# Kernel tuning notes

Measured on AMD Instinct MI355X. Metric: run time of the kernel, lower is better.

Reference implementation:

```python
import jax, jax.numpy as jnp
import numpy as np

B, S, D, H = 8, 4096, 512, 8
DK = D // H
DFF = 2 * D
KS = 3          # depthwise conv kernel size
EPS = 1e-6      # linear attention eps
LN_EPS = 1e-5


def setup_inputs() -> dict:
    key = jax.random.key(0)
    ks = jax.random.split(key, 24)
    w = lambda k, shape, s=0.02: (jax.random.normal(k, shape) * s).astype(jnp.float32)
    return {
        "x": jax.random.normal(ks[0], (B, S, D), dtype=jnp.float32),
        # q/k/v/o projections (torch Linear: y = x @ W.T + b, W is [out, in])
        "wq": w(ks[1], (D, D)), "bq": w(ks[2], (D,)),
        "wk": w(ks[3], (D, D)), "bk": w(ks[4], (D,)),
        "wv": w(ks[5], (D, D)), "bv": w(ks[6], (D,)),
        "wo": w(ks[7], (D, D)), "bo": w(ks[8], (D,)),
        # depthwise spatial convs on head_dim channels, weight [DK, KS], bias [DK]
        "qcw": w(ks[9], (DK, KS)), "qcb": w(ks[10], (DK,)),
        "kcw": w(ks[11], (DK, KS)), "kcb": w(ks[12], (DK,)),
        "vcw": w(ks[13], (DK, KS)), "vcb": w(ks[14], (DK,)),
        # conv-FFN 1x1 convs == linears, W1 [DFF, D], W2 [D, DFF]
        "w1": w(ks[15], (DFF, D)), "b1": w(ks[16], (DFF,)),
        "w2": w(ks[17], (D, DFF)), "b2": w(ks[18], (D,)),
        # layer norms
        "ln1_g": jnp.ones((D,), jnp.float32), "ln1_b": jnp.zeros((D,), jnp.float32),
        "ln2_g": jnp.ones((D,), jnp.float32), "ln2_b": jnp.zeros((D,), jnp.float32),
    }


def _sdwc(x, w, b):
    # x: [B, S, H, DK]; causal depthwise conv over seq per channel
    # (torch pads both sides by KS-1 then trims the last KS-1 => left pad only)
    s = x.shape[1]
    xp = jnp.pad(x, ((0, 0), (KS - 1, 0), (0, 0), (0, 0)))
    y = sum(xp[:, j:j + s] * w[:, j] for j in range(KS))
    return y + b


def _ln(x, g, b):
    m = jnp.mean(x, axis=-1, keepdims=True)
    v = jnp.mean((x - m) ** 2, axis=-1, keepdims=True)
    return (x - m) * jax.lax.rsqrt(v + LN_EPS) * g + b


def reference(x, wq, bq, wk, bk, wv, bv, qcw, qcb, kcw, kcb, vcw, vcb,
              wo, bo, w1, b1, w2, b2, ln1_g, ln1_b, ln2_g, ln2_b):
    b_, s_, _ = x.shape
    q = (jnp.einsum('bsd,od->bso', x, wq) + bq).reshape(b_, s_, H, DK)
    k = (jnp.einsum('bsd,od->bso', x, wk) + bk).reshape(b_, s_, H, DK)
    v = (jnp.einsum('bsd,od->bso', x, wv) + bv).reshape(b_, s_, H, DK)
    # depthwise spatial conv + elu(x)+1 feature map on q, k
    q = jax.nn.elu(_sdwc(q, qcw, qcb)) + 1.0
    k = jax.nn.elu(_sdwc(k, kcw, kcb)) + 1.0
    v = _sdwc(v, vcw, vcb)
    # linear attention in [B, H, S, DK]
    Q = q.transpose(0, 2, 1, 3)
    K = k.transpose(0, 2, 1, 3)
    V = v.transpose(0, 2, 1, 3)
    KV = jnp.einsum('bhsd,bhse->bhde', K, V)                       # [B,H,DK,DK]
    Z = 1.0 / jnp.einsum('bhsd,bhd->bhs', Q, K.sum(axis=2) + EPS)  # [B,H,S]
    Vn = jnp.einsum('bhde,bhsd,bhs->bhse', KV, Q, Z)               # [B,H,S,DK]
    attn = Vn.transpose(0, 2, 1, 3).reshape(b_, s_, D)
    attn = jnp.einsum('bsd,od->bso', attn, wo) + bo
    x = _ln(x + attn, ln1_g, ln1_b)
    # conv-FFN with squared (exact) GELU; dropout is identity at eval
    h = jnp.einsum('bsd,cd->bsc', x, w1) + b1
    g = jax.nn.gelu(h, approximate=False)
    h = g * g
    h = jnp.einsum('bsc,dc->bsd', h, w2) + b2
    return _ln(x + h, ln2_g, ln2_b)
```

## Files before the change

kernel.cpp:

```cpp
#include <hip/hip_runtime.h>
#include <hip/hip_bf16.h>
#include <math.h>

#define B_ 8
#define S_ 4096
#define D_ 512
#define H_ 8
#define DK_ 64
#define DFF_ 1024
#define SPLIT_ 16
#define KVSZ_ 4160
#define EPS_ 1e-6f
#define LN_EPS_ 1e-5f

typedef __attribute__((ext_vector_type(8))) short bf16x8;
typedef __attribute__((ext_vector_type(4))) float f32x4;

static __device__ __forceinline__ float b2f(unsigned short u) {
  unsigned int x = ((unsigned int)u) << 16;
  return __builtin_bit_cast(float, x);
}
static __device__ __forceinline__ unsigned short f2b(float f) {
  unsigned int u = __builtin_bit_cast(unsigned int, f);
  u += 0x7FFFu + ((u >> 16) & 1u);
  return (unsigned short)(u >> 16);
}

__global__ __launch_bounds__(256) void cvt_f32_bf16(
    const float* __restrict__ in, unsigned short* __restrict__ out, int n8)
{
  const int i = blockIdx.x * 256 + threadIdx.x;
  if (i >= n8) return;
  f32x4 a = ((const f32x4*)in)[i * 2];
  f32x4 b = ((const f32x4*)in)[i * 2 + 1];
  bf16x8 o;
  #pragma unroll
  for (int e = 0; e < 4; ++e) { o[e] = (short)f2b(a[e]); o[e + 4] = (short)f2b(b[e]); }
  ((bf16x8*)out)[i] = o;
}

__global__ __launch_bounds__(256) void cvt_weights(
    const float* __restrict__ wq, const float* __restrict__ wk,
    const float* __restrict__ wv, const float* __restrict__ wo,
    const float* __restrict__ w1, const float* __restrict__ w2,
    const float* __restrict__ bq, const float* __restrict__ bk,
    const float* __restrict__ bv,
    unsigned short* __restrict__ wb, float* __restrict__ bqkv)
{
  const int i = blockIdx.x * 256 + threadIdx.x;
  const float* src; int rel;
  if (i < 65536)       { src = (i < 32768)  ? wq : wk; rel = i & 32767; }
  else if (i < 131072) { src = (i < 98304)  ? wv : wo; rel = (i - 65536) & 32767; }
  else                 { src = (i < 196608) ? w1 : w2; rel = (i - 131072) & 65535; }
  f32x4 a = ((const f32x4*)src)[rel * 2];
  f32x4 b = ((const f32x4*)src)[rel * 2 + 1];
  bf16x8 o;
  #pragma unroll
  for (int e = 0; e < 4; ++e) { o[e] = (short)f2b(a[e]); o[e + 4] = (short)f2b(b[e]); }
  ((bf16x8*)wb)[i] = o;
  if (i < 1536) bqkv[i] = (i < 512) ? bq[i] : (i < 1024 ? bk[i - 512] : bv[i - 1024]);
}

template<int EPI>
__global__ __launch_bounds__(256, 2) void gemm_bt(
    const unsigned short* __restrict__ A,
    const unsigned short* __restrict__ W,
    const float* __restrict__ bias,
    unsigned short* __restrict__ C,
    int M, int N, int K, int ntx)
{
  __shared__ unsigned short sA[3 * 128 * 32];
  __shared__ unsigned short sB[3 * 256 * 32];
  const int t = threadIdx.x;
  const int wave = t >> 6;
  const int lane = t & 63;
  const int bid = blockIdx.x;
  const int logical = (bid & 7) * ((int)gridDim.x >> 3) + (bid >> 3);
  const int row0 = (logical / ntx) << 7;
  const int col0 = (logical % ntx) << 8;

  f32x4 acc[4][8] = {};

  const int srow = (wave << 4) + (lane >> 2);
  const int scol = (lane & 3) << 3;
  const unsigned short* ga = A + (size_t)(row0 + srow) * K + scol;
  const unsigned short* gb = W + (size_t)(col0 + srow) * K + scol;
  const int ldsoff = (wave << 9);

  const int wm = (wave >> 1) << 6;
  const int wn = (wave & 1) << 7;
  const int fr = lane & 15;
  const int fk = (lane >> 4) << 3;

  #define STAGE(bufsel, kt)                                                     \
    {                                                                           \
      _Pragma("unroll")                                                         \
      for (int i = 0; i < 2; ++i)                                               \
        __builtin_amdgcn_global_load_lds(                                       \
            (const __attribute__((address_space(1))) void*)(ga + (size_t)(i * 64) * K + (kt)), \
            (__attribute__((address_space(3))) void*)(sA + (bufsel) * 4096 + i * 2048 + ldsoff), \
            16, 0, 0);                                                          \
      _Pragma("unroll")                                                         \
      for (int i = 0; i < 4; ++i)                                               \
        __builtin_amdgcn_global_load_lds(                                       \
            (const __attribute__((address_space(1))) void*)(gb + (size_t)(i * 64) * K + (kt)), \
            (__attribute__((address_space(3))) void*)(sB + (bufsel) * 8192 + i * 2048 + ldsoff), \
            16, 0, 0);                                                          \
    }

  const int nt = K >> 5;
  STAGE(0, 0);
  STAGE(1, 32);

  int cur = 0, nxt = 2;
  for (int kt = 0; kt < nt; ++kt) {
    if (kt < nt - 1) asm volatile("s_waitcnt vmcnt(6)" ::: "memory");
    else             asm volatile("s_waitcnt vmcnt(0)" ::: "memory");
    __builtin_amdgcn_s_barrier();
    asm volatile("" ::: "memory");

    if (kt + 2 < nt) {
      STAGE(nxt, (kt + 2) * 32);
      nxt = (nxt == 2) ? 0 : nxt + 1;
    }

    const unsigned short* pA = sA + cur * 4096;
    const unsigned short* pB = sB + cur * 8192;
    bf16x8 af[4], bfv[8];
    #pragma unroll
    for (int i = 0; i < 4; ++i)
      af[i] = *(const bf16x8*)(pA + (wm + i * 16 + fr) * 32 + fk);
    #pragma unroll
    for (int j = 0; j < 8; ++j)
      bfv[j] = *(const bf16x8*)(pB + (wn + j * 16 + fr) * 32 + fk);
    #pragma unroll
    for (int i = 0; i < 4; ++i)
      #pragma unroll
      for (int j = 0; j < 8; ++j)
        acc[i][j] = __builtin_amdgcn_mfma_f32_16x16x32_bf16(af[i], bfv[j], acc[i][j], 0, 0, 0);

    cur = (cur == 2) ? 0 : cur + 1;
  }
  #undef STAGE

  const int crow0 = row0 + wm + ((lane >> 4) << 2);
  const int ccol0 = col0 + wn + fr;
  unsigned short* Cb = C;
  if (EPI == 2) Cb = C + (size_t)(col0 >> 9) * M * 512;
  const int cstride = (EPI == 2) ? 512 : N;
  #pragma unroll
  for (int j = 0; j < 8; ++j) {
    const int col = ccol0 + j * 16;
    const float bv = bias[col];
    const int lcol = (EPI == 2) ? (col & 511) : col;
    #pragma unroll
    for (int i = 0; i < 4; ++i) {
      #pragma unroll
      for (int r = 0; r < 4; ++r) {
        float v = acc[i][j][r] + bv;
        if (EPI == 1) {
          float g = 0.5f * v * (1.0f + erff(v * 0.70710678118654752f));
          v = g * g;
        }
        Cb[(size_t)(crow0 + i * 16 + r) * cstride + lcol] = f2b(v);
      }
    }
  }
}

template<bool ELUP1>
__global__ __launch_bounds__(256) void dwconv(
    const unsigned short* __restrict__ in,
    const float* __restrict__ cw,
    const float* __restrict__ cb,
    unsigned short* __restrict__ out)
{
  const int vid = blockIdx.x * 256 + threadIdx.x;
  const int d8 = vid & 63;
  const int bs = vid >> 6;
  const int s  = bs & (S_ - 1);
  const int d0 = d8 << 3;
  const int dk0 = d0 & 63;

  float acc[8], wf[3][8];
  #pragma unroll
  for (int i = 0; i < 8; ++i) acc[i] = cb[dk0 + i];
  #pragma unroll
  for (int j = 0; j < 3; ++j)
    #pragma unroll
    for (int i = 0; i < 8; ++i) wf[j][i] = cw[(dk0 + i) * 3 + j];

  const size_t base = (size_t)bs * D_ + d0;
  #pragma unroll
  for (int j = 0; j < 3; ++j) {
    const int sr = s - 2 + j;
    if (sr >= 0) {
      bf16x8 xv = *(const bf16x8*)(in + base - (size_t)(2 - j) * D_);
      #pragma unroll
      for (int i = 0; i < 8; ++i) acc[i] += wf[j][i] * b2f((unsigned short)xv[i]);
    }
  }
  bf16x8 ov;
  #pragma unroll
  for (int i = 0; i < 8; ++i) {
    float v = acc[i];
    if (ELUP1) v = (v > 0.0f) ? (v + 1.0f) : expf(v);
    ov[i] = (short)f2b(v);
  }
  *(bf16x8*)(out + base) = ov;
}

__global__ __launch_bounds__(256) void kv_partial(
    const unsigned short* __restrict__ kf,
    const unsigned short* __restrict__ vf,
    float* __restrict__ part)
{
  __shared__ unsigned short kc[16 * 64];
  __shared__ float vc[16 * 64];
  const int t = threadIdx.x;
  const int bh = blockIdx.x;
  const int b = bh >> 3, h = bh & 7;
  const int s0 = blockIdx.y * (S_ / SPLIT_);
  const int d = t >> 2;
  const int e0 = (t & 3) << 4;
  const int lr = (t & 127) >> 3;
  const int lc = (t & 7) << 3;

  float acc[16] = {};
  float ksum = 0.0f;

  for (int chunk = 0; chunk < S_ / SPLIT_; chunk += 16) {
    const size_t g = ((size_t)(b * S_ + s0 + chunk + lr)) * D_ + h * 64 + lc;
    if (t < 128) {
      *(bf16x8*)(kc + lr * 64 + lc) = *(const bf16x8*)(kf + g);
    } else {
      bf16x8 vv = *(const bf16x8*)(vf + g);
      #pragma unroll
      for (int i = 0; i < 8; ++i) vc[lr * 64 + lc + i] = b2f((unsigned short)vv[i]);
    }
    __syncthreads();
    #pragma unroll 4
    for (int ss = 0; ss < 16; ++ss) {
      const float kd = b2f(kc[ss * 64 + d]);
      ksum += kd;
      #pragma unroll
      for (int j = 0; j < 16; ++j) acc[j] += kd * vc[ss * 64 + e0 + j];
    }
    __syncthreads();
  }
  float* dst = part + ((size_t)bh * SPLIT_ + blockIdx.y) * KVSZ_;
  #pragma unroll
  for (int j = 0; j < 16; ++j) dst[d * 64 + e0 + j] = acc[j];
  if ((t & 3) == 0) dst[4096 + d] = ksum;
}

__global__ __launch_bounds__(256) void kv_finalize(
    const float* __restrict__ part, float* __restrict__ fin)
{
  const int bh = blockIdx.x;
  for (int idx = threadIdx.x; idx < KVSZ_; idx += 256) {
    float s = 0.0f;
    for (int p = 0; p < SPLIT_; ++p) s += part[((size_t)bh * SPLIT_ + p) * KVSZ_ + idx];
    if (idx >= 4096) s += EPS_;
    fin[(size_t)bh * KVSZ_ + idx] = s;
  }
}

__global__ __launch_bounds__(256) void attn_out(
    const unsigned short* __restrict__ qf,
    const float* __restrict__ fin,
    unsigned short* __restrict__ attn)
{
  __shared__ float kv[64 * 64];
  __shared__ float ks[64];
  const int t = threadIdx.x;
  const int bh = blockIdx.x, b = bh >> 3, h = bh & 7;
  const int s = blockIdx.y * 64 + (t >> 2);
  const int e0 = (t & 3) << 4;

  const float* src = fin + (size_t)bh * KVSZ_;
  for (int i = t; i < 4096; i += 256) kv[i] = src[i];
  if (t < 64) ks[t] = src[4096 + t];
  __syncthreads();

  const unsigned short* qrow = qf + ((size_t)(b * S_ + s)) * D_ + h * 64;
  float q[64];
  #pragma unroll
  for (int i = 0; i < 8; ++i) {
    bf16x8 qv = *(const bf16x8*)(qrow + i * 8);
    #pragma unroll
    for (int k = 0; k < 8; ++k) q[i * 8 + k] = b2f((unsigned short)qv[k]);
  }
  float zden = 0.0f;
  #pragma unroll
  for (int dd = 0; dd < 64; ++dd) zden += q[dd] * ks[dd];
  const float z = 1.0f / zden;

  float acc[16] = {};
  for (int dd = 0; dd < 64; ++dd) {
    const float qd = q[dd];
    #pragma unroll
    for (int j = 0; j < 16; ++j) acc[j] += qd * kv[dd * 64 + e0 + j];
  }
  unsigned short* orow = attn + ((size_t)(b * S_ + s)) * D_ + h * 64 + e0;
  bf16x8 o0, o1;
  #pragma unroll
  for (int j = 0; j < 8; ++j) { o0[j] = (short)f2b(acc[j] * z); o1[j] = (short)f2b(acc[8 + j] * z); }
  *(bf16x8*)(orow) = o0;
  *(bf16x8*)(orow + 8) = o1;
}

template<bool AF32, bool OF32>
__global__ __launch_bounds__(256) void ln_add(
    const void* __restrict__ xa_,
    const unsigned short* __restrict__ xb,
    const float* __restrict__ gg,
    const float* __restrict__ bb,
    void* __restrict__ out_)
{
  const int t = threadIdx.x, lane = t & 63, w = t >> 6;
  const size_t row = (size_t)blockIdx.x * 4 + w;
  const size_t base = row * D_ + lane * 8;

  float v[8];
  if (AF32) {
    const float* xa = (const float*)xa_;
    f32x4 a0 = *(const f32x4*)(xa + base);
    f32x4 a1 = *(const f32x4*)(xa + base + 4);
    #pragma unroll
    for (int i = 0; i < 4; ++i) { v[i] = a0[i]; v[i + 4] = a1[i]; }
  } else {
    bf16x8 a = *(const bf16x8*)((const unsigned short*)xa_ + base);
    #pragma unroll
    for (int i = 0; i < 8; ++i) v[i] = b2f((unsigned short)a[i]);
  }
  bf16x8 c = *(const bf16x8*)(xb + base);
  float sum = 0.0f;
  #pragma unroll
  for (int i = 0; i < 8; ++i) { v[i] += b2f((unsigned short)c[i]); sum += v[i]; }
  #pragma unroll
  for (int off = 1; off < 64; off <<= 1) sum += __shfl_xor(sum, off, 64);
  const float mean = sum * (1.0f / 512.0f);
  float sq = 0.0f;
  #pragma unroll
  for (int i = 0; i < 8; ++i) { const float dd = v[i] - mean; sq += dd * dd; }
  #pragma unroll
  for (int off = 1; off < 64; off <<= 1) sq += __shfl_xor(sq, off, 64);
  const float rstd = rsqrtf(sq * (1.0f / 512.0f) + LN_EPS_);

  if (OF32) {
    float* out = (float*)out_;
    f32x4 o0, o1;
    #pragma unroll
    for (int i = 0; i < 4; ++i) {
      o0[i] = (v[i] - mean) * rstd * gg[lane * 8 + i] + bb[lane * 8 + i];
      o1[i] = (v[i + 4] - mean) * rstd * gg[lane * 8 + i + 4] + bb[lane * 8 + i + 4];
    }
    *(f32x4*)(out + base) = o0;
    *(f32x4*)(out + base + 4) = o1;
  } else {
    unsigned short* out = (unsigned short*)out_;
    bf16x8 o;
    #pragma unroll
    for (int i = 0; i < 8; ++i)
      o[i] = (short)f2b((v[i] - mean) * rstd * gg[lane * 8 + i] + bb[lane * 8 + i]);
    *(bf16x8*)(out + base) = o;
  }
}

extern "C" void kernel_launch(void* const* d_in, const int* in_sizes, int n_in,
                              void* d_out, int out_size, void* d_ws, size_t ws_size,
                              hipStream_t stream) {
  const float* x    = (const float*)d_in[0];
  const float* wq   = (const float*)d_in[1];
  const float* bq   = (const float*)d_in[2];
  const float* wk   = (const float*)d_in[3];
  const float* bk   = (const float*)d_in[4];
  const float* wv   = (const float*)d_in[5];
  const float* bv   = (const float*)d_in[6];
  const float* wo   = (const float*)d_in[7];
  const float* bo   = (const float*)d_in[8];
  const float* qcw  = (const float*)d_in[9];
  const float* qcb  = (const float*)d_in[10];
  const float* kcw  = (const float*)d_in[11];
  const float* kcb  = (const float*)d_in[12];
  const float* vcw  = (const float*)d_in[13];
  const float* vcb  = (const float*)d_in[14];
  const float* w1   = (const float*)d_in[15];
  const float* b1   = (const float*)d_in[16];
  const float* w2   = (const float*)d_in[17];
  const float* b2   = (const float*)d_in[18];
  const float* ln1g = (const float*)d_in[19];
  const float* ln1b = (const float*)d_in[20];
  const float* ln2g = (const float*)d_in[21];
  const float* ln2b = (const float*)d_in[22];

  const size_t E = (size_t)B_ * S_ * D_;
  unsigned short* s0 = (unsigned short*)d_ws;
  unsigned short* s1 = s0 + E;
  unsigned short* s2 = s0 + 2 * E;
  unsigned short* s3 = s0 + 3 * E;
  float* part = (float*)s2;
  float* fin  = part + (size_t)64 * SPLIT_ * KVSZ_;

  unsigned short* wb = (unsigned short*)d_out;
  unsigned short* wqkv_b = wb;
  unsigned short* wo_b   = wb + 786432;
  unsigned short* w1_b   = wb + 1048576;
  unsigned short* w2_b   = wb + 1572864;
  float* bqkv = (float*)(wb + 2097152);

  const int M = B_ * S_;

  cvt_f32_bf16<<<(int)(E / 8 / 256), 256, 0, stream>>>(x, s3, (int)(E / 8));
  cvt_weights<<<1024, 256, 0, stream>>>(wq, wk, wv, wo, w1, w2, bq, bk, bv, wb, bqkv);

  gemm_bt<2><<<1536, 256, 0, stream>>>(s3, wqkv_b, bqkv, s0, M, 1536, D_, 6);
  dwconv<true ><<<M * 64 / 256, 256, 0, stream>>>(s0, qcw, qcb, s3);
  dwconv<true ><<<M * 64 / 256, 256, 0, stream>>>(s1, kcw, kcb, s0);
  dwconv<false><<<M * 64 / 256, 256, 0, stream>>>(s2, vcw, vcb, s1);
  kv_partial<<<dim3(B_ * H_, SPLIT_), 256, 0, stream>>>(s0, s1, part);
  kv_finalize<<<B_ * H_, 256, 0, stream>>>(part, fin);
  attn_out<<<dim3(B_ * H_, S_ / 64), 256, 0, stream>>>(s3, fin, s0);
  gemm_bt<0><<<512, 256, 0, stream>>>(s0, wo_b, bo, s1, M, D_, D_, 2);
  ln_add<true, false><<<M / 4, 256, 0, stream>>>(x, s1, ln1g, ln1b, s3);
  gemm_bt<1><<<1024, 256, 0, stream>>>(s3, w1_b, b1, s0, M, DFF_, D_, 4);
  gemm_bt<0><<<512, 256, 0, stream>>>(s0, w2_b, b2, s2, M, D_, DFF_, 2);
  ln_add<false, true><<<M / 4, 256, 0, stream>>>(s3, s2, ln2g, ln2b, d_out);
}
```

Baseline: 598.9 us.

## Fuse depthwise convs into KV and attention kernels, relax GEMM waitcnt

Removes the three standalone depthwise-conv kernels and recomputes the causal 3-tap conv (plus elu+1) inside kv_partial for K/V and inside attn_out for Q, reading pre-conv projections directly. This removes a full write and reread of three bf16 activation tensors, at the cost of loading two extra shifted rows per tile, which should mostly hit cache. The GEMM mainloop also moves its vmcnt wait to after issuing the next stage, allowing two stages in flight instead of one. Workspace buffers are reassigned so that the partial sums no longer overlap live data.

```diff
diff --git a/kernel.cpp b/kernel.cpp
--- a/kernel.cpp
+++ b/kernel.cpp
@@ -24,6 +24,9 @@
   unsigned int u = __builtin_bit_cast(unsigned int, f);
   u += 0x7FFFu + ((u >> 16) & 1u);
   return (unsigned short)(u >> 16);
+}
+static __device__ __forceinline__ float elu1(float v) {
+  return (v > 0.0f) ? (v + 1.0f) : expf(v);
 }
 
 __global__ __launch_bounds__(256) void cvt_f32_bf16(
@@ -114,14 +117,16 @@
 
   int cur = 0, nxt = 2;
   for (int kt = 0; kt < nt; ++kt) {
-    if (kt < nt - 1) asm volatile("s_waitcnt vmcnt(6)" ::: "memory");
-    else             asm volatile("s_waitcnt vmcnt(0)" ::: "memory");
     __builtin_amdgcn_s_barrier();
     asm volatile("" ::: "memory");
-
     if (kt + 2 < nt) {
       STAGE(nxt, (kt + 2) * 32);
       nxt = (nxt == 2) ? 0 : nxt + 1;
+      asm volatile("s_waitcnt vmcnt(12)" ::: "memory");
+    } else if (kt + 1 < nt) {
+      asm volatile("s_waitcnt vmcnt(6)" ::: "memory");
+    } else {
+      asm volatile("s_waitcnt vmcnt(0)" ::: "memory");
     }
 
     const unsigned short* pA = sA + cur * 4096;
@@ -168,54 +173,14 @@
   }
 }
 
-template<bool ELUP1>
-__global__ __launch_bounds__(256) void dwconv(
-    const unsigned short* __restrict__ in,
-    const float* __restrict__ cw,
-    const float* __restrict__ cb,
-    unsigned short* __restrict__ out)
-{
-  const int vid = blockIdx.x * 256 + threadIdx.x;
-  const int d8 = vid & 63;
-  const int bs = vid >> 6;
-  const int s  = bs & (S_ - 1);
-  const int d0 = d8 << 3;
-  const int dk0 = d0 & 63;
-
-  float acc[8], wf[3][8];
-  #pragma unroll
-  for (int i = 0; i < 8; ++i) acc[i] = cb[dk0 + i];
-  #pragma unroll
-  for (int j = 0; j < 3; ++j)
-    #pragma unroll
-    for (int i = 0; i < 8; ++i) wf[j][i] = cw[(dk0 + i) * 3 + j];
-
-  const size_t base = (size_t)bs * D_ + d0;
-  #pragma unroll
-  for (int j = 0; j < 3; ++j) {
-    const int sr = s - 2 + j;
-    if (sr >= 0) {
-      bf16x8 xv = *(const bf16x8*)(in + base - (size_t)(2 - j) * D_);
-      #pragma unroll
-      for (int i = 0; i < 8; ++i) acc[i] += wf[j][i] * b2f((unsigned short)xv[i]);
-    }
-  }
-  bf16x8 ov;
-  #pragma unroll
-  for (int i = 0; i < 8; ++i) {
-    float v = acc[i];
-    if (ELUP1) v = (v > 0.0f) ? (v + 1.0f) : expf(v);
-    ov[i] = (short)f2b(v);
-  }
-  *(bf16x8*)(out + base) = ov;
-}
-
 __global__ __launch_bounds__(256) void kv_partial(
-    const unsigned short* __restrict__ kf,
-    const unsigned short* __restrict__ vf,
+    const unsigned short* __restrict__ kp,
+    const unsigned short* __restrict__ vp,
+    const float* __restrict__ kcw, const float* __restrict__ kcb,
+    const float* __restrict__ vcw, const float* __restrict__ vcb,
     float* __restrict__ part)
 {
-  __shared__ unsigned short kc[16 * 64];
+  __shared__ float kc[16 * 64];
   __shared__ float vc[16 * 64];
   const int t = threadIdx.x;
   const int bh = blockIdx.x;
@@ -225,23 +190,43 @@
   const int e0 = (t & 3) << 4;
   const int lr = (t & 127) >> 3;
   const int lc = (t & 7) << 3;
+  const bool isv = t >= 128;
+
+  const float* cw = isv ? vcw : kcw;
+  const float* cb = isv ? vcb : kcb;
+  float w0[8], w1[8], w2[8], wb[8];
+  #pragma unroll
+  for (int i = 0; i < 8; ++i) {
+    w0[i] = cw[(lc + i) * 3 + 0];
+    w1[i] = cw[(lc + i) * 3 + 1];
+    w2[i] = cw[(lc + i) * 3 + 2];
+    wb[i] = cb[lc + i];
+  }
+  const unsigned short* src = isv ? vp : kp;
+  float* dstc = isv ? vc : kc;
 
   float acc[16] = {};
   float ksum = 0.0f;
 
   for (int chunk = 0; chunk < S_ / SPLIT_; chunk += 16) {
-    const size_t g = ((size_t)(b * S_ + s0 + chunk + lr)) * D_ + h * 64 + lc;
-    if (t < 128) {
-      *(bf16x8*)(kc + lr * 64 + lc) = *(const bf16x8*)(kf + g);
-    } else {
-      bf16x8 vv = *(const bf16x8*)(vf + g);
-      #pragma unroll
-      for (int i = 0; i < 8; ++i) vc[lr * 64 + lc + i] = b2f((unsigned short)vv[i]);
+    const int s = s0 + chunk + lr;
+    const size_t g = ((size_t)(b * S_ + s)) * D_ + h * 64 + lc;
+    bf16x8 r0 = *(const bf16x8*)(src + g);
+    bf16x8 r1 = {}, r2 = {};
+    if (s >= 1) r1 = *(const bf16x8*)(src + g - D_);
+    if (s >= 2) r2 = *(const bf16x8*)(src + g - 2 * D_);
+    #pragma unroll
+    for (int i = 0; i < 8; ++i) {
+      float v = w2[i] * b2f((unsigned short)r0[i])
+              + w1[i] * b2f((unsigned short)r1[i])
+              + w0[i] * b2f((unsigned short)r2[i]) + wb[i];
+      if (!isv) v = elu1(v);
+      dstc[lr * 64 + lc + i] = v;
     }
     __syncthreads();
     #pragma unroll 4
     for (int ss = 0; ss < 16; ++ss) {
-      const float kd = b2f(kc[ss * 64 + d]);
+      const float kd = kc[ss * 64 + d];
       ksum += kd;
       #pragma unroll
       for (int j = 0; j < 16; ++j) acc[j] += kd * vc[ss * 64 + e0 + j];
@@ -267,12 +252,15 @@
 }
 
 __global__ __launch_bounds__(256) void attn_out(
-    const unsigned short* __restrict__ qf,
+    const unsigned short* __restrict__ qp,
+    const float* __restrict__ qcw, const float* __restrict__ qcb,
     const float* __restrict__ fin,
     unsigned short* __restrict__ attn)
 {
   __shared__ float kv[64 * 64];
   __shared__ float ks[64];
+  __shared__ float qw[192];
+  __shared__ float qb[64];
   const int t = threadIdx.x;
   const int bh = blockIdx.x, b = bh >> 3, h = bh & 7;
   const int s = blockIdx.y * 64 + (t >> 2);
@@ -281,15 +269,26 @@
   const float* src = fin + (size_t)bh * KVSZ_;
   for (int i = t; i < 4096; i += 256) kv[i] = src[i];
   if (t < 64) ks[t] = src[4096 + t];
+  if (t < 192) qw[t] = qcw[t];
+  if (t < 64) qb[t] = qcb[t];
   __syncthreads();
 
-  const unsigned short* qrow = qf + ((size_t)(b * S_ + s)) * D_ + h * 64;
+  const unsigned short* qrow = qp + ((size_t)(b * S_ + s)) * D_ + h * 64;
   float q[64];
   #pragma unroll
-  for (int i = 0; i < 8; ++i) {
-    bf16x8 qv = *(const bf16x8*)(qrow + i * 8);
-    #pragma unroll
-    for (int k = 0; k < 8; ++k) q[i * 8 + k] = b2f((unsigned short)qv[k]);
+  for (int i8 = 0; i8 < 8; ++i8) {
+    bf16x8 a0 = *(const bf16x8*)(qrow + i8 * 8);
+    bf16x8 a1 = {}, a2 = {};
+    if (s >= 1) a1 = *(const bf16x8*)(qrow - D_ + i8 * 8);
+    if (s >= 2) a2 = *(const bf16x8*)(qrow - 2 * (size_t)D_ + i8 * 8);
+    #pragma unroll
+    for (int k = 0; k < 8; ++k) {
+      const int c = i8 * 8 + k;
+      float v = qw[c * 3 + 2] * b2f((unsigned short)a0[k])
+              + qw[c * 3 + 1] * b2f((unsigned short)a1[k])
+              + qw[c * 3 + 0] * b2f((unsigned short)a2[k]) + qb[c];
+      q[c] = elu1(v);
+    }
   }
   float zden = 0.0f;
   #pragma unroll
@@ -400,7 +399,7 @@
   unsigned short* s1 = s0 + E;
   unsigned short* s2 = s0 + 2 * E;
   unsigned short* s3 = s0 + 3 * E;
-  float* part = (float*)s2;
+  float* part = (float*)s3;
   float* fin  = part + (size_t)64 * SPLIT_ * KVSZ_;
 
   unsigned short* wb = (unsigned short*)d_out;
@@ -416,14 +415,11 @@
   cvt_weights<<<1024, 256, 0, stream>>>(wq, wk, wv, wo, w1, w2, bq, bk, bv, wb, bqkv);
 
   gemm_bt<2><<<1536, 256, 0, stream>>>(s3, wqkv_b, bqkv, s0, M, 1536, D_, 6);
-  dwconv<true ><<<M * 64 / 256, 256, 0, stream>>>(s0, qcw, qcb, s3);
-  dwconv<true ><<<M * 64 / 256, 256, 0, stream>>>(s1, kcw, kcb, s0);
-  dwconv<false><<<M * 64 / 256, 256, 0, stream>>>(s2, vcw, vcb, s1);
-  kv_partial<<<dim3(B_ * H_, SPLIT_), 256, 0, stream>>>(s0, s1, part);
+  kv_partial<<<dim3(B_ * H_, SPLIT_), 256, 0, stream>>>(s1, s2, kcw, kcb, vcw, vcb, part);
   kv_finalize<<<B_ * H_, 256, 0, stream>>>(part, fin);
-  attn_out<<<dim3(B_ * H_, S_ / 64), 256, 0, stream>>>(s3, fin, s0);
-  gemm_bt<0><<<512, 256, 0, stream>>>(s0, wo_b, bo, s1, M, D_, D_, 2);
-  ln_add<true, false><<<M / 4, 256, 0, stream>>>(x, s1, ln1g, ln1b, s3);
+  attn_out<<<dim3(B_ * H_, S_ / 64), 256, 0, stream>>>(s0, qcw, qcb, fin, s1);
+  gemm_bt<0><<<512, 256, 0, stream>>>(s1, wo_b, bo, s2, M, D_, D_, 2);
+  ln_add<true, false><<<M / 4, 256, 0, stream>>>(x, s2, ln1g, ln1b, s3);
   gemm_bt<1><<<1024, 256, 0, stream>>>(s3, w1_b, b1, s0, M, DFF_, D_, 4);
   gemm_bt<0><<<512, 256, 0, stream>>>(s0, w2_b, b2, s2, M, D_, DFF_, 2);
   ln_add<false, true><<<M / 4, 256, 0, stream>>>(s3, s2, ln2g, ln2b, d_out);
```

New measurement: 630.4 us. 5.3% more time.
